# Optimization experiments

Measured on AMD Instinct MI355X. Metric: run time of the kernel, lower is better.

The kernel has to match this reference:

```python
import jax, jax.numpy as jnp
import numpy as np

N_EMBED = 1024
HEAD_COUNT = 16
HEAD_SIZE = 64  # HEAD_COUNT * HEAD_SIZE == N_EMBED
SEQ = 2048
BATCH = 2


def setup_inputs() -> dict:
    key = jax.random.key(0)
    k_ix, k_q, k_k, k_v, k_p, k_b = jax.random.split(key, 6)
    scale = 1.0 / np.sqrt(N_EMBED)
    inp = {
        "ix": jax.random.normal(k_ix, (BATCH, SEQ, N_EMBED), dtype=jnp.float32),
        # per-head projection weights, stored as x @ W form: [H, C, D]
        "Wq": jax.random.normal(k_q, (HEAD_COUNT, N_EMBED, HEAD_SIZE), dtype=jnp.float32) * scale,
        "Wk": jax.random.normal(k_k, (HEAD_COUNT, N_EMBED, HEAD_SIZE), dtype=jnp.float32) * scale,
        "Wv": jax.random.normal(k_v, (HEAD_COUNT, N_EMBED, HEAD_SIZE), dtype=jnp.float32) * scale,
        # output projection (Linear with bias): y = x @ Wp + bp
        "Wp": jax.random.normal(k_p, (N_EMBED, N_EMBED), dtype=jnp.float32) * scale,
        "bp": jax.random.normal(k_b, (N_EMBED,), dtype=jnp.float32) * scale,
    }
    return inp


def reference(ix, Wq, Wk, Wv, Wp, bp):
    B, T, C = ix.shape
    # per-head projections: [B, H, T, D]
    Q = jnp.einsum("btc,hcd->bhtd", ix, Wq)
    K = jnp.einsum("btc,hcd->bhtd", ix, Wk)
    V = jnp.einsum("btc,hcd->bhtd", ix, Wv)
    # NOTE: faithful to source -- scores are MULTIPLIED by sqrt(C) (C = n_embed)
    scores = jnp.einsum("bhtd,bhsd->bhts", Q, K) * (C ** 0.5)
    causal = jnp.tril(jnp.ones((T, T), dtype=bool))
    scores = jnp.where(causal, scores, -jnp.inf)
    wei = jax.nn.softmax(scores, axis=-1)
    out = jnp.einsum("bhts,bhsd->bhtd", wei, V)
    # concat heads (matches torch.cat over per-head outputs along last dim)
    out = out.transpose(0, 2, 1, 3).reshape(B, T, -1)
    return out @ Wp + bp
```

## Files before the change

kernel.cpp:

```cpp
#include <hip/hip_runtime.h>

#define BATCH 2
#define SEQL  2048
#define NEMB  1024
#define NH    16
#define HD    64
#define MROWS (BATCH*SEQL)

#define QSCALE 46.166241308446828f

typedef short bf16x8 __attribute__((ext_vector_type(8)));
typedef float f32x16 __attribute__((ext_vector_type(16)));

__device__ __forceinline__ unsigned short f2bf(float x) {
    union { float f; unsigned u; } v; v.f = x;
    unsigned r = v.u + 0x7FFFu + ((v.u >> 16) & 1u);
    return (unsigned short)(r >> 16);
}
__device__ __forceinline__ void split_bf16(float x, unsigned short& hi, unsigned short& lo) {
    hi = f2bf(x);
    union { unsigned u; float f; } h; h.u = ((unsigned)hi) << 16;
    lo = f2bf(x - h.f);
}
__device__ __forceinline__ float bf2f(unsigned short b) {
    union { unsigned u; float f; } v; v.u = ((unsigned)b) << 16;
    return v.f;
}
__device__ __forceinline__ unsigned cvt_pk_bf16(float a, float b) {
    unsigned r;
    asm("v_cvt_pk_bf16_f32 %0, %1, %2" : "=v"(r) : "v"(a), "v"(b));
    return r;
}
__device__ __forceinline__ void plane_swap(unsigned& a, unsigned& b) {
    asm volatile("v_permlane32_swap_b32 %0, %1" : "+v"(a), "+v"(b));
}

__device__ __forceinline__ int slot16(int chunk, int lane) {
    return chunk * 66 + (lane & 31) + 33 * (lane >> 5);
}

__global__ __launch_bounds__(256) void split_convert_kernel(
    const float* __restrict__ src,
    unsigned short* __restrict__ dhi, unsigned short* __restrict__ dlo)
{
    int i = (blockIdx.x * 256 + threadIdx.x) * 4;
    float4 v = *(const float4*)(src + i);
    unsigned short h[4], l[4];
    split_bf16(v.x, h[0], l[0]); split_bf16(v.y, h[1], l[1]);
    split_bf16(v.z, h[2], l[2]); split_bf16(v.w, h[3], l[3]);
    uint2 ph, pl;
    ph.x = h[0] | ((unsigned)h[1] << 16); ph.y = h[2] | ((unsigned)h[3] << 16);
    pl.x = l[0] | ((unsigned)l[1] << 16); pl.y = l[2] | ((unsigned)l[3] << 16);
    *(uint2*)(dhi + i) = ph;
    *(uint2*)(dlo + i) = pl;
}

__global__ __launch_bounds__(256) void transpose_convert_kernel(
    const float* __restrict__ Wq, const float* __restrict__ Wk,
    const float* __restrict__ Wv, const float* __restrict__ Wp,
    unsigned short* __restrict__ qhi, unsigned short* __restrict__ qlo,
    unsigned short* __restrict__ khi, unsigned short* __restrict__ klo,
    unsigned short* __restrict__ vhi, unsigned short* __restrict__ pt)
{
    __shared__ float tile[64][68];
    const int z = blockIdx.z, hb = blockIdx.y, c0 = blockIdx.x * 64;
    const float* src; int rstride; unsigned short* dhi; unsigned short* dlo;
    if (z == 0)      { src = Wq + (size_t)hb * 65536; rstride = 64;   dhi = qhi; dlo = qlo; }
    else if (z == 1) { src = Wk + (size_t)hb * 65536; rstride = 64;   dhi = khi; dlo = klo; }
    else if (z == 2) { src = Wv + (size_t)hb * 65536; rstride = 64;   dhi = vhi; dlo = nullptr; }
    else             { src = Wp + (size_t)hb * 64;    rstride = 1024; dhi = pt;  dlo = nullptr; }
    const int tid = threadIdx.x;
    #pragma unroll
    for (int i = 0; i < 4; ++i) {
        int fidx = i * 256 + tid;
        int r  = fidx >> 4;
        int dq = (fidx & 15) * 4;
        float4 v = *(const float4*)(src + (size_t)(c0 + r) * rstride + dq);
        *(float4*)&tile[r][dq] = v;
    }
    __syncthreads();
    #pragma unroll
    for (int i = 0; i < 4; ++i) {
        int fidx = i * 256 + tid;
        int d  = fidx >> 4;
        int cq = (fidx & 15) * 4;
        size_t base = (size_t)(hb * 64 + d) * 1024 + c0 + cq;
        unsigned short hh[4], ll[4];
        #pragma unroll
        for (int j = 0; j < 4; ++j) split_bf16(tile[cq + j][d], hh[j], ll[j]);
        uint2 ph; ph.x = hh[0] | ((unsigned)hh[1] << 16); ph.y = hh[2] | ((unsigned)hh[3] << 16);
        *(uint2*)(dhi + base) = ph;
        if (dlo) {
            uint2 pl; pl.x = ll[0] | ((unsigned)ll[1] << 16); pl.y = ll[2] | ((unsigned)ll[3] << 16);
            *(uint2*)(dlo + base) = pl;
        }
    }
}

__global__ __launch_bounds__(256, 2) void qkv_gemm(
    const unsigned short* __restrict__ Ahi, const unsigned short* __restrict__ Alo,
    const unsigned short* __restrict__ Bq_hi, const unsigned short* __restrict__ Bq_lo,
    const unsigned short* __restrict__ Bk_hi, const unsigned short* __restrict__ Bk_lo,
    const unsigned short* __restrict__ Bv_hi,
    unsigned short* __restrict__ Qhi, unsigned short* __restrict__ Qlo,
    unsigned short* __restrict__ Khi, unsigned short* __restrict__ Klo,
    unsigned short* __restrict__ Vt)
{
    __shared__ unsigned short smem[2][4][4224];

    const int bid = blockIdx.x;
    const int z   = bid % 3;
    const int xy  = bid / 3;
    const int m0  = (xy & 31) * 128;
    const int n0  = (xy >> 5) * 128;

    const bool split = (z < 2);
    const unsigned short* __restrict__ Bhi = (z == 0) ? Bq_hi : (z == 1) ? Bk_hi : Bv_hi;
    const unsigned short* __restrict__ Blo = (z == 0) ? Bq_lo : Bk_lo;
    unsigned short* __restrict__ Ohi = (z == 0) ? Qhi : Khi;
    unsigned short* __restrict__ Olo = (z == 0) ? Qlo : Klo;
    const float oscale = (z == 0) ? QSCALE : 1.0f;

    const int tid  = threadIdx.x;
    const int wid  = tid >> 6, lane = tid & 63;
    const int wr   = wid >> 1, wc = wid & 1;

    int roff_[2], slot_[2];
    #pragma unroll
    for (int q = 0; q < 2; ++q) {
        int f   = q * 256 + tid;
        int row = f >> 2;
        int k8  = (f & 3) * 8;
        roff_[q] = row * 1024 + k8;
        slot_[q] = slot16((row >> 5) * 2 + (k8 >> 4), (row & 31) + 32 * ((k8 >> 3) & 1)) * 8;
    }
    const unsigned short* __restrict__ Ah = Ahi + (size_t)m0 * 1024;
    const unsigned short* __restrict__ Bh = Bhi + (size_t)n0 * 1024;
    const unsigned short* __restrict__ Al = split ? Alo + (size_t)m0 * 1024 : Ahi;
    const unsigned short* __restrict__ Bl = split ? Blo + (size_t)n0 * 1024 : Bhi;

    bf16x8 pah[2], pbh[2], pal[2], pbl[2];

    #define LOADT(KK)  do { _Pragma("unroll")                                   \
        for (int q = 0; q < 2; ++q) {                                           \
            pah[q] = *(const bf16x8*)(Ah + roff_[q] + (KK));                    \
            pbh[q] = *(const bf16x8*)(Bh + roff_[q] + (KK));                    \
            if (split) {                                                        \
                pal[q] = *(const bf16x8*)(Al + roff_[q] + (KK));                \
                pbl[q] = *(const bf16x8*)(Bl + roff_[q] + (KK));                \
            }                                                                   \
        } } while (0)

    #define WRITET(NB) do { _Pragma("unroll")                                   \
        for (int q = 0; q < 2; ++q) {                                           \
            *(bf16x8*)(&smem[NB][0][slot_[q]]) = pah[q];                        \
            *(bf16x8*)(&smem[NB][1][slot_[q]]) = pbh[q];                        \
            if (split) {                                                        \
                *(bf16x8*)(&smem[NB][2][slot_[q]]) = pal[q];                    \
                *(bf16x8*)(&smem[NB][3][slot_[q]]) = pbl[q];                    \
            }                                                                   \
        } } while (0)

    f32x16 acc[2][2] = {};

    LOADT(0);
    WRITET(0);
    LOADT(32);

    for (int t = 0; t < 32; ++t) {
        __syncthreads();
        if (t + 1 < 32) {
            WRITET((t + 1) & 1);
            if (t + 2 < 32) LOADT((t + 2) * 32);
        }
        const int cb = t & 1;
        const unsigned short* a_hi = smem[cb][0];
        const unsigned short* b_hi = smem[cb][1];
        const unsigned short* a_lo = smem[cb][2];
        const unsigned short* b_lo = smem[cb][3];

        #pragma unroll
        for (int kch = 0; kch < 2; ++kch) {
            bf16x8 ah[2], bh_[2];
            #pragma unroll
            for (int mt = 0; mt < 2; ++mt)
                ah[mt] = *(const bf16x8*)(a_hi + slot16((2 * wr + mt) * 2 + kch, lane) * 8);
            #pragma unroll
            for (int nt = 0; nt < 2; ++nt)
                bh_[nt] = *(const bf16x8*)(b_hi + slot16((2 * wc + nt) * 2 + kch, lane) * 8);
            if (split) {
                bf16x8 al[2], bl[2];
                #pragma unroll
                for (int mt = 0; mt < 2; ++mt)
                    al[mt] = *(const bf16x8*)(a_lo + slot16((2 * wr + mt) * 2 + kch, lane) * 8);
                #pragma unroll
                for (int nt = 0; nt < 2; ++nt)
                    bl[nt] = *(const bf16x8*)(b_lo + slot16((2 * wc + nt) * 2 + kch, lane) * 8);
                #pragma unroll
                for (int mt = 0; mt < 2; ++mt)
                    #pragma unroll
                    for (int nt = 0; nt < 2; ++nt) {
                        acc[mt][nt] = __builtin_amdgcn_mfma_f32_32x32x16_bf16(ah[mt], bh_[nt], acc[mt][nt], 0, 0, 0);
                        acc[mt][nt] = __builtin_amdgcn_mfma_f32_32x32x16_bf16(ah[mt], bl[nt],  acc[mt][nt], 0, 0, 0);
                        acc[mt][nt] = __builtin_amdgcn_mfma_f32_32x32x16_bf16(al[mt], bh_[nt], acc[mt][nt], 0, 0, 0);
                    }
            } else {
                #pragma unroll
                for (int mt = 0; mt < 2; ++mt)
                    #pragma unroll
                    for (int nt = 0; nt < 2; ++nt)
                        acc[mt][nt] = __builtin_amdgcn_mfma_f32_32x32x16_bf16(bh_[nt], ah[mt], acc[mt][nt], 0, 0, 0);
            }
        }
    }
    #undef LOADT
    #undef WRITET

    #pragma unroll
    for (int mt = 0; mt < 2; ++mt) {
        #pragma unroll
        for (int nt = 0; nt < 2; ++nt) {
            if (z == 2) {
                const int mcol = m0 + wr * 64 + mt * 32 + (lane & 31);
                const int bb = mcol >> 11, tt = mcol & (SEQL - 1);
                #pragma unroll
                for (int r = 0; r < 16; ++r) {
                    int nrow = n0 + wc * 64 + nt * 32 + (r & 3) + 8 * (r >> 2) + 4 * (lane >> 5);
                    int head = nrow >> 6, dd = nrow & 63;
                    Vt[((size_t)(bb * NH + head) * HD + dd) * SEQL + tt] = f2bf(acc[mt][nt][r]);
                }
            } else {
                const int ncol = n0 + wc * 64 + nt * 32 + (lane & 31);
                const int head = ncol >> 6, d = ncol & 63;
                #pragma unroll
                for (int r = 0; r < 16; ++r) {
                    int mrow = m0 + wr * 64 + mt * 32 + (r & 3) + 8 * (r >> 2) + 4 * (lane >> 5);
                    int bb = mrow >> 11, t = mrow & (SEQL - 1);
                    size_t idx = ((size_t)(bb * NH + head) * SEQL + t) * HD + d;
                    float v = acc[mt][nt][r] * oscale;
                    unsigned short hi = f2bf(v);
                    Ohi[idx] = hi;
                    union { unsigned u; float f; } hf; hf.u = ((unsigned)hi) << 16;
                    Olo[idx] = f2bf(v - hf.f);
                }
            }
        }
    }
}

__global__ __launch_bounds__(256) void attn_mfma_kernel(
    const unsigned short* __restrict__ Qhi, const unsigned short* __restrict__ Qlo,
    const unsigned short* __restrict__ Khi, const unsigned short* __restrict__ Klo,
    const unsigned short* __restrict__ Vt,
    unsigned short* __restrict__ Op0, unsigned short* __restrict__ Op1,
    float* __restrict__ Ml)
{
    __shared__ unsigned short smem[2][3][4224];

    const int bid  = blockIdx.x;
    const int xcd  = bid & 7;
    const int idx  = bid >> 3;
    const int bh   = xcd * 4 + (idx & 3);
    const int rest = idx >> 2;
    const int j    = 15 - (rest >> 1);
    const int sp   = rest & 1;

    const int tid  = threadIdx.x;
    const int wid  = tid >> 6;
    const int lane = tid & 63;
    const int ln   = lane & 31;
    const int h    = lane >> 5;

    const int qb_idx = 4 * j + wid;
    const int qb     = qb_idx * 32;
    const int qglob  = qb + ln;
    const int cutoff = 2 * j + (wid >> 1);
    const int tbeg   = sp ? (j + 1) : 0;
    const int tend   = sp ? (2 * j + 2) : (j + 1);

    const unsigned short* __restrict__ Qbh = Qhi + (size_t)bh * SEQL * HD;
    const unsigned short* __restrict__ Qbl = Qlo + (size_t)bh * SEQL * HD;
    const unsigned short* __restrict__ Kbh = Khi + (size_t)bh * SEQL * HD;
    const unsigned short* __restrict__ Kbl = Klo + (size_t)bh * SEQL * HD;
    const unsigned short* __restrict__ Vtb = Vt  + (size_t)bh * HD * SEQL;

    bf16x8 qhi[4], qlo[4];
    #pragma unroll
    for (int c = 0; c < 4; ++c) {
        qhi[c] = *(const bf16x8*)(Qbh + (size_t)qglob * HD + c * 16 + h * 8);
        qlo[c] = *(const bf16x8*)(Qbl + (size_t)qglob * HD + c * 16 + h * 8);
    }

    int s_[2], d8_[2], ks_[2];
    #pragma unroll
    for (int ff = 0; ff < 2; ++ff) {
        int fidx = ff * 256 + tid;
        s_[ff]  = fidx >> 3;
        d8_[ff] = fidx & 7;
        ks_[ff] = slot16((s_[ff] >> 5) * 4 + (d8_[ff] >> 1),
                         (s_[ff] & 31) + 32 * (d8_[ff] & 1)) * 8;
    }

    bf16x8 kh[2], kl[2], vv[2];
    {
        const int s0p = tbeg * 64;
        #pragma unroll
        for (int ff = 0; ff < 2; ++ff) {
            kh[ff] = *(const bf16x8*)(Kbh + (size_t)(s0p + s_[ff]) * HD + d8_[ff] * 8);
            kl[ff] = *(const bf16x8*)(Kbl + (size_t)(s0p + s_[ff]) * HD + d8_[ff] * 8);
            vv[ff] = *(const bf16x8*)(Vtb + (size_t)s_[ff] * SEQL + s0p + d8_[ff] * 8);
        }
        const int pb = tbeg & 1;
        #pragma unroll
        for (int ff = 0; ff < 2; ++ff) {
            *(bf16x8*)(&smem[pb][0][ks_[ff]]) = kh[ff];
            *(bf16x8*)(&smem[pb][1][ks_[ff]]) = kl[ff];
            *(bf16x8*)(&smem[pb][2][ks_[ff]]) = vv[ff];
        }
        if (tbeg + 1 < tend) {
            const int s0n = (tbeg + 1) * 64;
            #pragma unroll
            for (int ff = 0; ff < 2; ++ff) {
                kh[ff] = *(const bf16x8*)(Kbh + (size_t)(s0n + s_[ff]) * HD + d8_[ff] * 8);
                kl[ff] = *(const bf16x8*)(Kbl + (size_t)(s0n + s_[ff]) * HD + d8_[ff] * 8);
                vv[ff] = *(const bf16x8*)(Vtb + (size_t)s_[ff] * SEQL + s0n + d8_[ff] * 8);
            }
        }
    }

    f32x16 oacc[2] = {};
    float m_run = -1e30f, l_run = 0.f;

    for (int t = tbeg; t < tend; ++t) {
        __syncthreads();
        if (t + 1 < tend) {
            const int nb = (t + 1) & 1;
            #pragma unroll
            for (int ff = 0; ff < 2; ++ff) {
                *(bf16x8*)(&smem[nb][0][ks_[ff]]) = kh[ff];
                *(bf16x8*)(&smem[nb][1][ks_[ff]]) = kl[ff];
                *(bf16x8*)(&smem[nb][2][ks_[ff]]) = vv[ff];
            }
            if (t + 2 < tend) {
                const int s0n = (t + 2) * 64;
                #pragma unroll
                for (int ff = 0; ff < 2; ++ff) {
                    kh[ff] = *(const bf16x8*)(Kbh + (size_t)(s0n + s_[ff]) * HD + d8_[ff] * 8);
                    kl[ff] = *(const bf16x8*)(Kbl + (size_t)(s0n + s_[ff]) * HD + d8_[ff] * 8);
                    vv[ff] = *(const bf16x8*)(Vtb + (size_t)s_[ff] * SEQL + s0n + d8_[ff] * 8);
                }
            }
        }

        if (t <= cutoff) {
            const int cb = t & 1;
            const int s0 = t * 64;
            const bf16x8* khf = (const bf16x8*)&smem[cb][0][0];
            const bf16x8* klf = (const bf16x8*)&smem[cb][1][0];
            const bf16x8* vtf = (const bf16x8*)&smem[cb][2][0];

            f32x16 sacc[2] = {};
            __builtin_amdgcn_s_setprio(1);
            #pragma unroll
            for (int sb = 0; sb < 2; ++sb) {
                #pragma unroll
                for (int c = 0; c < 4; ++c) {
                    bf16x8 ah = khf[slot16(sb * 4 + c, lane)];
                    bf16x8 al = klf[slot16(sb * 4 + c, lane)];
                    sacc[sb] = __builtin_amdgcn_mfma_f32_32x32x16_bf16(ah, qhi[c], sacc[sb], 0, 0, 0);
                    sacc[sb] = __builtin_amdgcn_mfma_f32_32x32x16_bf16(ah, qlo[c], sacc[sb], 0, 0, 0);
                    sacc[sb] = __builtin_amdgcn_mfma_f32_32x32x16_bf16(al, qhi[c], sacc[sb], 0, 0, 0);
                }
            }
            __builtin_amdgcn_s_setprio(0);

            if ((s0 + 63) > qb) {
                #pragma unroll
                for (int sb = 0; sb < 2; ++sb)
                    #pragma unroll
                    for (int r = 0; r < 16; ++r) {
                        int srow = (r & 3) + 8 * (r >> 2) + 4 * h + sb * 32;
                        if ((s0 + srow) > qglob) sacc[sb][r] = -1e30f;
                    }
            }

            float mtile = -1e30f;
            #pragma unroll
            for (int sb = 0; sb < 2; ++sb)
                #pragma unroll
                for (int r = 0; r < 16; ++r)
                    mtile = fmaxf(mtile, sacc[sb][r]);
            mtile = fmaxf(mtile, __shfl_xor(mtile, 32));

            if (!__all(mtile - m_run <= 11.5f)) {
                const float mnew  = fmaxf(m_run, mtile);
                const float alpha = exp2f(m_run - mnew);
                l_run *= alpha;
                #pragma unroll
                for (int dt = 0; dt < 2; ++dt)
                    #pragma unroll
                    for (int r = 0; r < 16; ++r)
                        oacc[dt][r] *= alpha;
                m_run = mnew;
            }

            float ps0 = 0.f, ps1 = 0.f;
            unsigned pw[2][8];
            #pragma unroll
            for (int sb = 0; sb < 2; ++sb) {
                #pragma unroll
                for (int r2 = 0; r2 < 8; ++r2) {
                    float p0 = exp2f(sacc[sb][2 * r2]     - m_run);
                    float p1 = exp2f(sacc[sb][2 * r2 + 1] - m_run);
                    if (sb == 0) ps0 += p0 + p1; else ps1 += p0 + p1;
                    pw[sb][r2] = cvt_pk_bf16(p0, p1);
                }
            }
            float psum = ps0 + ps1;
            psum += __shfl_xor(psum, 32);
            l_run += psum;

            bf16x8 pfrag[4];
            #pragma unroll
            for (int sb = 0; sb < 2; ++sb) {
                #pragma unroll
                for (int c = 0; c < 2; ++c) {
                    unsigned u0 = pw[sb][4 * c + 0], u2 = pw[sb][4 * c + 2];
                    unsigned u1 = pw[sb][4 * c + 1], u3 = pw[sb][4 * c + 3];
                    plane_swap(u0, u2);
                    plane_swap(u1, u3);
                    union { unsigned u[4]; bf16x8 v; } cvt;
                    cvt.u[0] = u0; cvt.u[1] = u1; cvt.u[2] = u2; cvt.u[3] = u3;
                    pfrag[sb * 2 + c] = cvt.v;
                }
            }

            __builtin_amdgcn_s_setprio(1);
            #pragma unroll
            for (int dt = 0; dt < 2; ++dt)
                #pragma unroll
                for (int sc = 0; sc < 4; ++sc)
                    oacc[dt] = __builtin_amdgcn_mfma_f32_32x32x16_bf16(
                        vtf[slot16(dt * 4 + sc, lane)], pfrag[sc], oacc[dt], 0, 0, 0);
            __builtin_amdgcn_s_setprio(0);
        }
    }

    unsigned short* op = (sp ? Op1 : Op0)
        + ((size_t)(bh >> 4) * SEQL + qglob) * NEMB + (bh & 15) * HD;
    #pragma unroll
    for (int dt = 0; dt < 2; ++dt) {
        #pragma unroll
        for (int rg = 0; rg < 4; ++rg) {
            int d0 = dt * 32 + rg * 8 + h * 4;
            uint2 w;
            w.x = cvt_pk_bf16(oacc[dt][rg * 4 + 0], oacc[dt][rg * 4 + 1]);
            w.y = cvt_pk_bf16(oacc[dt][rg * 4 + 2], oacc[dt][rg * 4 + 3]);
            *(uint2*)(op + d0) = w;
        }
    }
    if (h == 0) {
        float2 mlv; mlv.x = m_run; mlv.y = l_run;
        *(float2*)(Ml + ((size_t)(sp * 32 + bh) * SEQL + qglob) * 2) = mlv;
    }
}

__global__ __launch_bounds__(256) void attn_merge_kernel(
    unsigned short* __restrict__ Op0, const unsigned short* __restrict__ Op1,
    const float* __restrict__ Ml)
{
    const int gid  = blockIdx.x * 256 + threadIdx.x;
    const int row  = gid >> 7;
    const int col  = (gid & 127) * 8;
    const int bh   = ((row >> 11) << 4) + (col >> 6);
    const int q    = row & (SEQL - 1);

    float2 ml0 = *(const float2*)(Ml + ((size_t)bh * SEQL + q) * 2);
    float2 ml1 = *(const float2*)(Ml + ((size_t)(32 + bh) * SEQL + q) * 2);
    const float M  = fmaxf(ml0.x, ml1.x);
    const float w0 = exp2f(ml0.x - M);
    const float w1 = exp2f(ml1.x - M);
    const float rd = 1.0f / (ml0.y * w0 + ml1.y * w1);
    const float f0 = w0 * rd, f1 = w1 * rd;

    size_t off = (size_t)row * NEMB + col;
    uint4 a = *(const uint4*)(Op0 + off);
    uint4 b = *(const uint4*)(Op1 + off);
    const unsigned short* ap = (const unsigned short*)&a;
    const unsigned short* bp = (const unsigned short*)&b;
    uint4 o;
    unsigned* opw = (unsigned*)&o;
    #pragma unroll
    for (int i = 0; i < 4; ++i) {
        float r0 = bf2f(ap[2*i])     * f0 + bf2f(bp[2*i])     * f1;
        float r1 = bf2f(ap[2*i + 1]) * f0 + bf2f(bp[2*i + 1]) * f1;
        opw[i] = cvt_pk_bf16(r0, r1);
    }
    *(uint4*)(Op0 + off) = o;
}

__global__ __launch_bounds__(256, 2) void out_proj_kernel(
    const unsigned short* __restrict__ A, const unsigned short* __restrict__ B,
    const float* __restrict__ bias, float* __restrict__ out)
{
    __shared__ unsigned short smem[2][2][4224];

    const int m0 = blockIdx.x * 128;
    const int n0 = blockIdx.y * 128;
    const int tid  = threadIdx.x;
    const int wid  = tid >> 6, lane = tid & 63;
    const int wr   = wid >> 1, wc = wid & 1;

    int roff_[2], slot_[2];
    #pragma unroll
    for (int q = 0; q < 2; ++q) {
        int f   = q * 256 + tid;
        int row = f >> 2;
        int k8  = (f & 3) * 8;
        roff_[q] = row * 1024 + k8;
        slot_[q] = slot16((row >> 5) * 2 + (k8 >> 4), (row & 31) + 32 * ((k8 >> 3) & 1)) * 8;
    }
    const unsigned short* __restrict__ Ab = A + (size_t)m0 * 1024;
    const unsigned short* __restrict__ Bb = B + (size_t)n0 * 1024;

    bf16x8 pa[2], pb[2];
    #pragma unroll
    for (int q = 0; q < 2; ++q) {
        pa[q] = *(const bf16x8*)(Ab + roff_[q]);
        pb[q] = *(const bf16x8*)(Bb + roff_[q]);
    }
    #pragma unroll
    for (int q = 0; q < 2; ++q) {
        *(bf16x8*)(&smem[0][0][slot_[q]]) = pa[q];
        *(bf16x8*)(&smem[0][1][slot_[q]]) = pb[q];
    }
    #pragma unroll
    for (int q = 0; q < 2; ++q) {
        pa[q] = *(const bf16x8*)(Ab + roff_[q] + 32);
        pb[q] = *(const bf16x8*)(Bb + roff_[q] + 32);
    }

    f32x16 acc[2][2] = {};

    for (int t = 0; t < 32; ++t) {
        __syncthreads();
        if (t + 1 < 32) {
            const int nb = (t + 1) & 1;
            #pragma unroll
            for (int q = 0; q < 2; ++q) {
                *(bf16x8*)(&smem[nb][0][slot_[q]]) = pa[q];
                *(bf16x8*)(&smem[nb][1][slot_[q]]) = pb[q];
            }
            if (t + 2 < 32) {
                #pragma unroll
                for (int q = 0; q < 2; ++q) {
                    pa[q] = *(const bf16x8*)(Ab + roff_[q] + (t + 2) * 32);
                    pb[q] = *(const bf16x8*)(Bb + roff_[q] + (t + 2) * 32);
                }
            }
        }
        const int cb = t & 1;
        const unsigned short* a_s = smem[cb][0];
        const unsigned short* b_s = smem[cb][1];
        #pragma unroll
        for (int kch = 0; kch < 2; ++kch) {
            bf16x8 ah[2], bh_[2];
            #pragma unroll
            for (int mt = 0; mt < 2; ++mt)
                ah[mt] = *(const bf16x8*)(a_s + slot16((2 * wr + mt) * 2 + kch, lane) * 8);
            #pragma unroll
            for (int nt = 0; nt < 2; ++nt)
                bh_[nt] = *(const bf16x8*)(b_s + slot16((2 * wc + nt) * 2 + kch, lane) * 8);
            #pragma unroll
            for (int mt = 0; mt < 2; ++mt)
                #pragma unroll
                for (int nt = 0; nt < 2; ++nt)
                    acc[mt][nt] = __builtin_amdgcn_mfma_f32_32x32x16_bf16(ah[mt], bh_[nt], acc[mt][nt], 0, 0, 0);
        }
    }

    #pragma unroll
    for (int mt = 0; mt < 2; ++mt) {
        #pragma unroll
        for (int nt = 0; nt < 2; ++nt) {
            const int ncol = n0 + wc * 64 + nt * 32 + (lane & 31);
            const float bv = bias[ncol];
            #pragma unroll
            for (int r = 0; r < 16; ++r) {
                int mrow = m0 + wr * 64 + mt * 32 + (r & 3) + 8 * (r >> 2) + 4 * (lane >> 5);
                out[(size_t)mrow * 1024 + ncol] = acc[mt][nt][r] + bv;
            }
        }
    }
}

extern "C" void kernel_launch(void* const* d_in, const int* in_sizes, int n_in,
                              void* d_out, int out_size, void* d_ws, size_t ws_size,
                              hipStream_t stream)
{
    const float* ix = (const float*)d_in[0];
    const float* Wq = (const float*)d_in[1];
    const float* Wk = (const float*)d_in[2];
    const float* Wv = (const float*)d_in[3];
    const float* Wp = (const float*)d_in[4];
    const float* bp = (const float*)d_in[5];
    float* out = (float*)d_out;

    char* ws = (char*)d_ws;
    #define WSOFF(mb) ((unsigned short*)(ws + (size_t)(mb) * 1024 * 1024))
    unsigned short* ix_hi  = WSOFF(0);
    unsigned short* ix_lo  = WSOFF(8);
    unsigned short* Wqt_hi = WSOFF(16);
    unsigned short* Wqt_lo = WSOFF(18);
    unsigned short* Wkt_hi = WSOFF(20);
    unsigned short* Wkt_lo = WSOFF(22);
    unsigned short* Wvt_hi = WSOFF(24);
    unsigned short* Qhi    = WSOFF(26);
    unsigned short* Qlo    = WSOFF(34);
    unsigned short* Khi    = WSOFF(42);
    unsigned short* Klo    = WSOFF(50);
    unsigned short* Wpt    = WSOFF(58);
    unsigned short* Op0    = WSOFF(0);
    unsigned short* Op1    = WSOFF(8);
    float*          Ml     = (float*)WSOFF(16);
    unsigned short* Vt     = (unsigned short*)d_out;
    #undef WSOFF

    split_convert_kernel<<<MROWS * NEMB / 4 / 256, 256, 0, stream>>>(ix, ix_hi, ix_lo);
    transpose_convert_kernel<<<dim3(16, 16, 4), 256, 0, stream>>>(
        Wq, Wk, Wv, Wp, Wqt_hi, Wqt_lo, Wkt_hi, Wkt_lo, Wvt_hi, Wpt);
    qkv_gemm<<<768, 256, 0, stream>>>(
        ix_hi, ix_lo, Wqt_hi, Wqt_lo, Wkt_hi, Wkt_lo, Wvt_hi,
        Qhi, Qlo, Khi, Klo, Vt);
    attn_mfma_kernel<<<1024, 256, 0, stream>>>(Qhi, Qlo, Khi, Klo, Vt, Op0, Op1, Ml);
    attn_merge_kernel<<<MROWS * NEMB / 8 / 256, 256, 0, stream>>>(Op0, Op1, Ml);
    out_proj_kernel<<<dim3(MROWS / 128, NEMB / 128), 256, 0, stream>>>(Op0, Wpt, bp, out);
}
```

Before: 197.2 us.

## Merge convert kernels and rebalance QKV GEMM with separate V tiling

```diff
diff --git a/kernel.cpp b/kernel.cpp
--- a/kernel.cpp
+++ b/kernel.cpp
@@ -39,37 +39,43 @@
     return chunk * 66 + (lane & 31) + 33 * (lane >> 5);
 }
 
-__global__ __launch_bounds__(256) void split_convert_kernel(
-    const float* __restrict__ src,
-    unsigned short* __restrict__ dhi, unsigned short* __restrict__ dlo)
-{
-    int i = (blockIdx.x * 256 + threadIdx.x) * 4;
-    float4 v = *(const float4*)(src + i);
-    unsigned short h[4], l[4];
-    split_bf16(v.x, h[0], l[0]); split_bf16(v.y, h[1], l[1]);
-    split_bf16(v.z, h[2], l[2]); split_bf16(v.w, h[3], l[3]);
-    uint2 ph, pl;
-    ph.x = h[0] | ((unsigned)h[1] << 16); ph.y = h[2] | ((unsigned)h[3] << 16);
-    pl.x = l[0] | ((unsigned)l[1] << 16); pl.y = l[2] | ((unsigned)l[3] << 16);
-    *(uint2*)(dhi + i) = ph;
-    *(uint2*)(dlo + i) = pl;
-}
-
-__global__ __launch_bounds__(256) void transpose_convert_kernel(
+__global__ __launch_bounds__(256) void convert_kernel(
+    const float* __restrict__ ixsrc,
     const float* __restrict__ Wq, const float* __restrict__ Wk,
     const float* __restrict__ Wv, const float* __restrict__ Wp,
+    unsigned short* __restrict__ ixhi, unsigned short* __restrict__ ixlo,
     unsigned short* __restrict__ qhi, unsigned short* __restrict__ qlo,
     unsigned short* __restrict__ khi, unsigned short* __restrict__ klo,
     unsigned short* __restrict__ vhi, unsigned short* __restrict__ pt)
 {
     __shared__ float tile[64][68];
-    const int z = blockIdx.z, hb = blockIdx.y, c0 = blockIdx.x * 64;
+    const int bid = blockIdx.x;
+    const int tid = threadIdx.x;
+
+    if (bid < 4096) {
+        int i = (bid * 256 + tid) * 4;
+        float4 v = *(const float4*)(ixsrc + i);
+        unsigned short h[4], l[4];
+        split_bf16(v.x, h[0], l[0]); split_bf16(v.y, h[1], l[1]);
+        split_bf16(v.z, h[2], l[2]); split_bf16(v.w, h[3], l[3]);
+        uint2 ph, pl;
+        ph.x = h[0] | ((unsigned)h[1] << 16); ph.y = h[2] | ((unsigned)h[3] << 16);
+        pl.x = l[0] | ((unsigned)l[1] << 16); pl.y = l[2] | ((unsigned)l[3] << 16);
+        *(uint2*)(ixhi + i) = ph;
+        *(uint2*)(ixlo + i) = pl;
+        return;
+    }
+
+    const int t  = bid - 4096;
+    const int z  = t >> 8;
+    const int rem = t & 255;
+    const int hb = (rem >> 4) & 15;
+    const int c0 = (rem & 15) * 64;
     const float* src; int rstride; unsigned short* dhi; unsigned short* dlo;
     if (z == 0)      { src = Wq + (size_t)hb * 65536; rstride = 64;   dhi = qhi; dlo = qlo; }
     else if (z == 1) { src = Wk + (size_t)hb * 65536; rstride = 64;   dhi = khi; dlo = klo; }
     else if (z == 2) { src = Wv + (size_t)hb * 65536; rstride = 64;   dhi = vhi; dlo = nullptr; }
     else             { src = Wp + (size_t)hb * 64;    rstride = 1024; dhi = pt;  dlo = nullptr; }
-    const int tid = threadIdx.x;
     #pragma unroll
     for (int i = 0; i < 4; ++i) {
         int fidx = i * 256 + tid;
@@ -109,93 +115,84 @@
     __shared__ unsigned short smem[2][4][4224];
 
     const int bid = blockIdx.x;
-    const int z   = bid % 3;
-    const int xy  = bid / 3;
-    const int m0  = (xy & 31) * 128;
-    const int n0  = (xy >> 5) * 128;
-
-    const bool split = (z < 2);
-    const unsigned short* __restrict__ Bhi = (z == 0) ? Bq_hi : (z == 1) ? Bk_hi : Bv_hi;
-    const unsigned short* __restrict__ Blo = (z == 0) ? Bq_lo : Bk_lo;
-    unsigned short* __restrict__ Ohi = (z == 0) ? Qhi : Khi;
-    unsigned short* __restrict__ Olo = (z == 0) ? Qlo : Klo;
-    const float oscale = (z == 0) ? QSCALE : 1.0f;
-
     const int tid  = threadIdx.x;
     const int wid  = tid >> 6, lane = tid & 63;
     const int wr   = wid >> 1, wc = wid & 1;
 
-    int roff_[2], slot_[2];
-    #pragma unroll
-    for (int q = 0; q < 2; ++q) {
-        int f   = q * 256 + tid;
-        int row = f >> 2;
-        int k8  = (f & 3) * 8;
-        roff_[q] = row * 1024 + k8;
-        slot_[q] = slot16((row >> 5) * 2 + (k8 >> 4), (row & 31) + 32 * ((k8 >> 3) & 1)) * 8;
-    }
-    const unsigned short* __restrict__ Ah = Ahi + (size_t)m0 * 1024;
-    const unsigned short* __restrict__ Bh = Bhi + (size_t)n0 * 1024;
-    const unsigned short* __restrict__ Al = split ? Alo + (size_t)m0 * 1024 : Ahi;
-    const unsigned short* __restrict__ Bl = split ? Blo + (size_t)n0 * 1024 : Bhi;
-
-    bf16x8 pah[2], pbh[2], pal[2], pbl[2];
-
-    #define LOADT(KK)  do { _Pragma("unroll")                                   \
-        for (int q = 0; q < 2; ++q) {                                           \
-            pah[q] = *(const bf16x8*)(Ah + roff_[q] + (KK));                    \
-            pbh[q] = *(const bf16x8*)(Bh + roff_[q] + (KK));                    \
-            if (split) {                                                        \
+    if (bid < 512) {
+        const int z   = bid >> 8;
+        const int xy  = bid & 255;
+        const int m0  = (xy & 31) * 128;
+        const int n0  = (xy >> 5) * 128;
+        const unsigned short* __restrict__ Bhi = z ? Bk_hi : Bq_hi;
+        const unsigned short* __restrict__ Blo = z ? Bk_lo : Bq_lo;
+        unsigned short* __restrict__ Ohi = z ? Khi : Qhi;
+        unsigned short* __restrict__ Olo = z ? Klo : Qlo;
+        const float oscale = z ? 1.0f : QSCALE;
+
+        int roff_[2], slot_[2];
+        #pragma unroll
+        for (int q = 0; q < 2; ++q) {
+            int f   = q * 256 + tid;
+            int row = f >> 2;
+            int k8  = (f & 3) * 8;
+            roff_[q] = row * 1024 + k8;
+            slot_[q] = slot16((row >> 5) * 2 + (k8 >> 4), (row & 31) + 32 * ((k8 >> 3) & 1)) * 8;
+        }
+        const unsigned short* __restrict__ Ah = Ahi + (size_t)m0 * 1024;
+        const unsigned short* __restrict__ Bh = Bhi + (size_t)n0 * 1024;
+        const unsigned short* __restrict__ Al = Alo + (size_t)m0 * 1024;
+        const unsigned short* __restrict__ Bl = Blo + (size_t)n0 * 1024;
+
+        bf16x8 pah[2], pbh[2], pal[2], pbl[2];
+
+        #define LOADT(KK)  do { _Pragma("unroll")                               \
+            for (int q = 0; q < 2; ++q) {                                       \
+                pah[q] = *(const bf16x8*)(Ah + roff_[q] + (KK));                \
+                pbh[q] = *(const bf16x8*)(Bh + roff_[q] + (KK));                \
                 pal[q] = *(const bf16x8*)(Al + roff_[q] + (KK));                \
                 pbl[q] = *(const bf16x8*)(Bl + roff_[q] + (KK));                \
-            }                                                                   \
-        } } while (0)
-
-    #define WRITET(NB) do { _Pragma("unroll")                                   \
-        for (int q = 0; q < 2; ++q) {                                           \
-            *(bf16x8*)(&smem[NB][0][slot_[q]]) = pah[q];                        \
-            *(bf16x8*)(&smem[NB][1][slot_[q]]) = pbh[q];                        \
-            if (split) {                                                        \
+            } } while (0)
+
+        #define WRITET(NB) do { _Pragma("unroll")                               \
+            for (int q = 0; q < 2; ++q) {                                       \
+                *(bf16x8*)(&smem[NB][0][slot_[q]]) = pah[q];                    \
+                *(bf16x8*)(&smem[NB][1][slot_[q]]) = pbh[q];                    \
                 *(bf16x8*)(&smem[NB][2][slot_[q]]) = pal[q];                    \
                 *(bf16x8*)(&smem[NB][3][slot_[q]]) = pbl[q];                    \
-            }                                                                   \
-        } } while (0)
-
-    f32x16 acc[2][2] = {};
-
-    LOADT(0);
-    WRITET(0);
-    LOADT(32);
-
-    for (int t = 0; t < 32; ++t) {
-        __syncthreads();
-        if (t + 1 < 32) {
-            WRITET((t + 1) & 1);
-            if (t + 2 < 32) LOADT((t + 2) * 32);
-        }
-        const int cb = t & 1;
-        const unsigned short* a_hi = smem[cb][0];
-        const unsigned short* b_hi = smem[cb][1];
-        const unsigned short* a_lo = smem[cb][2];
-        const unsigned short* b_lo = smem[cb][3];
-
-        #pragma unroll
-        for (int kch = 0; kch < 2; ++kch) {
-            bf16x8 ah[2], bh_[2];
-            #pragma unroll
-            for (int mt = 0; mt < 2; ++mt)
-                ah[mt] = *(const bf16x8*)(a_hi + slot16((2 * wr + mt) * 2 + kch, lane) * 8);
-            #pragma unroll
-            for (int nt = 0; nt < 2; ++nt)
-                bh_[nt] = *(const bf16x8*)(b_hi + slot16((2 * wc + nt) * 2 + kch, lane) * 8);
-            if (split) {
-                bf16x8 al[2], bl[2];
-                #pragma unroll
-                for (int mt = 0; mt < 2; ++mt)
+            } } while (0)
+
+        f32x16 acc[2][2] = {};
+
+        LOADT(0);
+        WRITET(0);
+        LOADT(32);
+
+        for (int t = 0; t < 32; ++t) {
+            __syncthreads();
+            if (t + 1 < 32) {
+                WRITET((t + 1) & 1);
+                if (t + 2 < 32) LOADT((t + 2) * 32);
+            }
+            const int cb = t & 1;
+            const unsigned short* a_hi = smem[cb][0];
+            const unsigned short* b_hi = smem[cb][1];
+            const unsigned short* a_lo = smem[cb][2];
+            const unsigned short* b_lo = smem[cb][3];
+
+            #pragma unroll
+            for (int kch = 0; kch < 2; ++kch) {
+                bf16x8 ah[2], bh_[2], al[2], bl[2];
+                #pragma unroll
+                for (int mt = 0; mt < 2; ++mt) {
+                    ah[mt] = *(const bf16x8*)(a_hi + slot16((2 * wr + mt) * 2 + kch, lane) * 8);
                     al[mt] = *(const bf16x8*)(a_lo + slot16((2 * wr + mt) * 2 + kch, lane) * 8);
-                #pragma unroll
-                for (int nt = 0; nt < 2; ++nt)
-                    bl[nt] = *(const bf16x8*)(b_lo + slot16((2 * wc + nt) * 2 + kch, lane) * 8);
+                }
+                #pragma unroll
+                for (int nt = 0; nt < 2; ++nt) {
+                    bh_[nt] = *(const bf16x8*)(b_hi + slot16((2 * wc + nt) * 2 + kch, lane) * 8);
+                    bl[nt]  = *(const bf16x8*)(b_lo + slot16((2 * wc + nt) * 2 + kch, lane) * 8);
+                }
                 #pragma unroll
                 for (int mt = 0; mt < 2; ++mt)
                     #pragma unroll
@@ -204,45 +201,104 @@
                         acc[mt][nt] = __builtin_amdgcn_mfma_f32_32x32x16_bf16(ah[mt], bl[nt],  acc[mt][nt], 0, 0, 0);
                         acc[mt][nt] = __builtin_amdgcn_mfma_f32_32x32x16_bf16(al[mt], bh_[nt], acc[mt][nt], 0, 0, 0);
                     }
-            } else {
-                #pragma unroll
-                for (int mt = 0; mt < 2; ++mt)
-                    #pragma unroll
-                    for (int nt = 0; nt < 2; ++nt)
-                        acc[mt][nt] = __builtin_amdgcn_mfma_f32_32x32x16_bf16(bh_[nt], ah[mt], acc[mt][nt], 0, 0, 0);
-            }
-        }
-    }
-    #undef LOADT
-    #undef WRITET
-
-    #pragma unroll
-    for (int mt = 0; mt < 2; ++mt) {
-        #pragma unroll
-        for (int nt = 0; nt < 2; ++nt) {
-            if (z == 2) {
-                const int mcol = m0 + wr * 64 + mt * 32 + (lane & 31);
-                const int bb = mcol >> 11, tt = mcol & (SEQL - 1);
-                #pragma unroll
-                for (int r = 0; r < 16; ++r) {
-                    int nrow = n0 + wc * 64 + nt * 32 + (r & 3) + 8 * (r >> 2) + 4 * (lane >> 5);
-                    int head = nrow >> 6, dd = nrow & 63;
-                    Vt[((size_t)(bb * NH + head) * HD + dd) * SEQL + tt] = f2bf(acc[mt][nt][r]);
-                }
-            } else {
+            }
+        }
+        #undef LOADT
+        #undef WRITET
+
+        #pragma unroll
+        for (int mt = 0; mt < 2; ++mt) {
+            #pragma unroll
+            for (int nt = 0; nt < 2; ++nt) {
                 const int ncol = n0 + wc * 64 + nt * 32 + (lane & 31);
                 const int head = ncol >> 6, d = ncol & 63;
                 #pragma unroll
                 for (int r = 0; r < 16; ++r) {
                     int mrow = m0 + wr * 64 + mt * 32 + (r & 3) + 8 * (r >> 2) + 4 * (lane >> 5);
-                    int bb = mrow >> 11, t = mrow & (SEQL - 1);
-                    size_t idx = ((size_t)(bb * NH + head) * SEQL + t) * HD + d;
+                    int bb = mrow >> 11, tt = mrow & (SEQL - 1);
+                    size_t idx = ((size_t)(bb * NH + head) * SEQL + tt) * HD + d;
                     float v = acc[mt][nt][r] * oscale;
                     unsigned short hi = f2bf(v);
                     Ohi[idx] = hi;
                     union { unsigned u; float f; } hf; hf.u = ((unsigned)hi) << 16;
                     Olo[idx] = f2bf(v - hf.f);
                 }
+            }
+        }
+    } else {
+        const int vid = bid - 512;
+        const int m0  = (vid >> 4) * 128;
+        const int n0  = (vid & 15) * 64;
+
+        int roffA_[2], slotA_[2], roffB, slotB;
+        #pragma unroll
+        for (int q = 0; q < 2; ++q) {
+            int f   = q * 256 + tid;
+            int row = f >> 2;
+            int k8  = (f & 3) * 8;
+            roffA_[q] = row * 1024 + k8;
+            slotA_[q] = slot16((row >> 5) * 2 + (k8 >> 4), (row & 31) + 32 * ((k8 >> 3) & 1)) * 8;
+        }
+        {
+            int row = tid >> 2;
+            int k8  = (tid & 3) * 8;
+            roffB  = row * 1024 + k8;
+            slotB  = slot16((row >> 5) * 2 + (k8 >> 4), (row & 31) + 32 * ((k8 >> 3) & 1)) * 8;
+        }
+        const unsigned short* __restrict__ Ah = Ahi + (size_t)m0 * 1024;
+        const unsigned short* __restrict__ Bh = Bv_hi + (size_t)n0 * 1024;
+
+        bf16x8 pa[2], pb;
+        #pragma unroll
+        for (int q = 0; q < 2; ++q) pa[q] = *(const bf16x8*)(Ah + roffA_[q]);
+        pb = *(const bf16x8*)(Bh + roffB);
+        #pragma unroll
+        for (int q = 0; q < 2; ++q) *(bf16x8*)(&smem[0][0][slotA_[q]]) = pa[q];
+        *(bf16x8*)(&smem[0][1][slotB]) = pb;
+        #pragma unroll
+        for (int q = 0; q < 2; ++q) pa[q] = *(const bf16x8*)(Ah + roffA_[q] + 32);
+        pb = *(const bf16x8*)(Bh + roffB + 32);
+
+        f32x16 acc[2] = {};
+
+        for (int t = 0; t < 32; ++t) {
+            __syncthreads();
+            if (t + 1 < 32) {
+                const int nb = (t + 1) & 1;
+                #pragma unroll
+                for (int q = 0; q < 2; ++q) *(bf16x8*)(&smem[nb][0][slotA_[q]]) = pa[q];
+                *(bf16x8*)(&smem[nb][1][slotB]) = pb;
+                if (t + 2 < 32) {
+                    #pragma unroll
+                    for (int q = 0; q < 2; ++q) pa[q] = *(const bf16x8*)(Ah + roffA_[q] + (t + 2) * 32);
+                    pb = *(const bf16x8*)(Bh + roffB + (t + 2) * 32);
+                }
+            }
+            const int cb = t & 1;
+            const unsigned short* a_s = smem[cb][0];
+            const unsigned short* b_s = smem[cb][1];
+            #pragma unroll
+            for (int kch = 0; kch < 2; ++kch) {
+                bf16x8 ah[2], bh_;
+                #pragma unroll
+                for (int mt = 0; mt < 2; ++mt)
+                    ah[mt] = *(const bf16x8*)(a_s + slot16((2 * wr + mt) * 2 + kch, lane) * 8);
+                bh_ = *(const bf16x8*)(b_s + slot16(wc * 2 + kch, lane) * 8);
+                #pragma unroll
+                for (int mt = 0; mt < 2; ++mt)
+                    acc[mt] = __builtin_amdgcn_mfma_f32_32x32x16_bf16(bh_, ah[mt], acc[mt], 0, 0, 0);
+            }
+        }
+
+        #pragma unroll
+        for (int mt = 0; mt < 2; ++mt) {
+            const int mcol = m0 + wr * 64 + mt * 32 + (lane & 31);
+            const int bb = mcol >> 11, tt = mcol & (SEQL - 1);
+            #pragma unroll
+            for (int r = 0; r < 16; ++r) {
+                int nrow = n0 + wc * 32 + (r & 3) + 8 * (r >> 2) + 4 * (lane >> 5);
+                int head = nrow >> 6, dd = nrow & 63;
+                Vt[((size_t)(bb * NH + head) * HD + dd) * SEQL + tt] = f2bf(acc[mt][r]);
             }
         }
     }
@@ -626,10 +682,10 @@
     unsigned short* Vt     = (unsigned short*)d_out;
     #undef WSOFF
 
-    split_convert_kernel<<<MROWS * NEMB / 4 / 256, 256, 0, stream>>>(ix, ix_hi, ix_lo);
-    transpose_convert_kernel<<<dim3(16, 16, 4), 256, 0, stream>>>(
-        Wq, Wk, Wv, Wp, Wqt_hi, Wqt_lo, Wkt_hi, Wkt_lo, Wvt_hi, Wpt);
-    qkv_gemm<<<768, 256, 0, stream>>>(
+    convert_kernel<<<5120, 256, 0, stream>>>(
+        ix, Wq, Wk, Wv, Wp, ix_hi, ix_lo,
+        Wqt_hi, Wqt_lo, Wkt_hi, Wkt_lo, Wvt_hi, Wpt);
+    qkv_gemm<<<1024, 256, 0, stream>>>(
         ix_hi, ix_lo, Wqt_hi, Wqt_lo, Wkt_hi, Wkt_lo, Wvt_hi,
         Qhi, Qlo, Khi, Klo, Vt);
     attn_mfma_kernel<<<1024, 256, 0, stream>>>(Qhi, Qlo, Khi, Klo, Vt, Op0, Op1, Ml);
```

Measured after the change: 173.2 us, median of 3. 12.2% less time.
